# Kernel optimization log

Hardware: AMD Instinct MI355X
Metric: run time of the kernel (lower is better)

## Reference

```python
import jax, jax.numpy as jnp
import numpy as np

B, S, D = 256, 512, 128
NQ, NC, NQD, NCD = 20000, 2000, 101, 101


def setup_inputs() -> dict:
    key = jax.random.key(0)
    ks = jax.random.split(key, 32)
    s = 0.05
    inp = {
        "question_seq": jax.random.randint(ks[0], (B, S), 0, NQ),
        "concept_seq": jax.random.randint(ks[1], (B, S), 0, NC),
        "question_diff_seq": jax.random.randint(ks[2], (B, S), 0, NQD),
        "concept_diff_seq": jax.random.randint(ks[3], (B, S), 0, NCD),
        "correct_seq": jax.random.randint(ks[4], (B, S), 0, 2),
        "E_q": jax.random.normal(ks[5], (NQ, D)) * s,
        "E_c": jax.random.normal(ks[6], (NC, D)) * s,
        "E_qd": jax.random.normal(ks[7], (NQD, D)) * s,
        "E_cd": jax.random.normal(ks[8], (NCD, D)) * s,
        "E_corr": jax.random.normal(ks[9], (2, D)) * s,
        "Wx": jax.random.normal(ks[10], (4 * D, D)) * s,
        "bx": jnp.zeros((D,)),
        "W_s1": jax.random.normal(ks[11], (D, D)) * s,
        "b_s1": jnp.zeros((D,)),
        "W_s2": jax.random.normal(ks[12], (D, D)) * s,
        "b_s2": jnp.zeros((D,)),
        "W_p1": jax.random.normal(ks[13], (2 * D, D)) * s,
        "b_p1": jnp.zeros((D,)),
        "W_p2": jax.random.normal(ks[14], (2 * D, D)) * s,
        "b_p2": jnp.zeros((D,)),
        "W_ki": jax.random.normal(ks[15], (4 * D, D)) * s,
        "b_ki": jnp.zeros((D,)),
        # xavier_uniform init of h_pre: bound = sqrt(6/(fan_in+fan_out))
        "h0": jax.random.uniform(ks[16], (B, D), minval=-1.0, maxval=1.0) * np.sqrt(6.0 / (B + D)),
    }
    return inp


def reference(question_seq, concept_seq, question_diff_seq, concept_diff_seq,
              correct_seq, E_q, E_c, E_qd, E_cd, E_corr,
              Wx, bx, W_s1, b_s1, W_s2, b_s2,
              W_p1, b_p1, W_p2, b_p2, W_ki, b_ki, h0):
    # embedding lookups: [B,S,D] each
    q = E_q[question_seq]
    c = E_c[concept_seq]
    qd = E_qd[question_diff_seq]
    cd = E_cd[concept_diff_seq]
    corr = E_corr[correct_seq]
    # generate_x_MLP applied to full sequence at once (loop-invariant)
    x = jnp.concatenate([q, c, qd, cd], axis=-1) @ Wx + bx  # [B,S,D]
    # time-major inputs for the recurrence over t = 0..S-2
    xs = jnp.swapaxes(x, 0, 1)          # [S,B,D]
    corr_t = jnp.swapaxes(corr, 0, 1)   # [S,B,D]
    qd_t = jnp.swapaxes(qd, 0, 1)
    cd_t = jnp.swapaxes(cd, 0, 1)

    def step(h, inp):
        x_t, x_next, co, qdt, cdt = inp
        d = x_t - h
        sdf = jax.nn.sigmoid(d @ W_s1 + b_s1) * jnp.tanh(d @ W_s2 + b_s2)  # dropout=eval
        pk_in = jnp.concatenate([sdf, co], axis=-1)
        pka = jax.nn.sigmoid(pk_in @ W_p1 + b_p1) * jnp.tanh(pk_in @ W_p2 + b_p2)
        ki_in = jnp.concatenate([h, co, qdt, cdt], axis=-1)
        g = jax.nn.sigmoid(ki_in @ W_ki + b_ki)
        h_new = g * h + (1.0 - g) * pka
        y_t = jax.nn.sigmoid(jnp.sum(x_next * h_new, axis=-1))  # [B]
        return h_new, y_t

    scan_in = (xs[:-1], xs[1:], corr_t[:-1], qd_t[:-1], cd_t[:-1])
    _, y_body = jax.lax.scan(step, h0, scan_in)  # y_body: [S-1,B]
    y = jnp.concatenate([y_body.T, jnp.zeros((question_seq.shape[0], 1), y_body.dtype)], axis=1)
    return y  # [B,S], last column zero as in original
```

## Files before the change

### kernel.cpp

```cpp
#include <hip/hip_runtime.h>

#define BB 256
#define SS 512
#define DD 128

__device__ __forceinline__ float sigf(float v) {
    return __builtin_amdgcn_rcpf(1.0f + __expf(-v));
}
__device__ __forceinline__ float tanhf_(float v) {
    return 1.0f - 2.0f * __builtin_amdgcn_rcpf(__expf(2.0f * v) + 1.0f);
}

__device__ __forceinline__ void lds_barrier() {
    asm volatile("s_waitcnt lgkmcnt(0)" ::: "memory");
    __builtin_amdgcn_s_barrier();
    __builtin_amdgcn_sched_barrier(0);
}

typedef _Float16 f16x2 __attribute__((ext_vector_type(2)));
typedef _Float16 f16x8 __attribute__((ext_vector_type(8)));
typedef float    f32x4 __attribute__((ext_vector_type(4)));

#define MFMA16(A, B, C) __builtin_amdgcn_mfma_f32_16x16x32_f16((A), (B), (C), 0, 0, 0)

#define N_EQ  (20000 * 128)
#define N_EC  (2000 * 128)
#define N_EQD (101 * 128)
#define N_ECD (101 * 128)
#define N_WXT (512 * 128)
#define N_WS  (128 * 128)
#define N_CVT (N_EQ + N_EC + N_EQD + N_ECD + N_WXT + 2 * N_WS)

__global__ __launch_bounds__(256) void dimkt_cvt(
    const float* __restrict__ E_q, const float* __restrict__ E_c,
    const float* __restrict__ E_qd, const float* __restrict__ E_cd,
    const float* __restrict__ Wx,
    const float* __restrict__ W_s1, const float* __restrict__ W_s2,
    _Float16* __restrict__ E_qh, _Float16* __restrict__ E_ch,
    _Float16* __restrict__ E_qdh, _Float16* __restrict__ E_cdh,
    _Float16* __restrict__ WxTh,
    _Float16* __restrict__ Ws1T, _Float16* __restrict__ Ws2T)
{
    int o = blockIdx.x * 256 + threadIdx.x;
    if (o >= N_CVT) return;
    if (o < N_EQ) { E_qh[o] = (_Float16)E_q[o]; return; }
    o -= N_EQ;
    if (o < N_EC) { E_ch[o] = (_Float16)E_c[o]; return; }
    o -= N_EC;
    if (o < N_EQD) { E_qdh[o] = (_Float16)E_qd[o]; return; }
    o -= N_EQD;
    if (o < N_ECD) { E_cdh[o] = (_Float16)E_cd[o]; return; }
    o -= N_ECD;
    if (o < N_WXT) {
        int n = o >> 9, k = o & 511;
        WxTh[o] = (_Float16)Wx[k * 128 + n];
        return;
    }
    o -= N_WXT;
    if (o < N_WS) {
        int n = o >> 7, k = o & 127;
        Ws1T[o] = (_Float16)W_s1[k * 128 + n];
        return;
    }
    o -= N_WS;
    {
        int n = o >> 7, k = o & 127;
        Ws2T[o] = (_Float16)W_s2[k * 128 + n];
    }
}

__global__ void dimkt_tables(const float* __restrict__ E_corr,
                             const float* __restrict__ E_qd,
                             const float* __restrict__ E_cd,
                             const float* __restrict__ W_ki,
                             const float* __restrict__ W_p1,
                             const float* __restrict__ W_p2,
                             const float* __restrict__ b_ki,
                             const float* __restrict__ b_p1,
                             const float* __restrict__ b_p2,
                             float* __restrict__ Ck, float* __restrict__ Cp1,
                             float* __restrict__ Cp2, float* __restrict__ Qk,
                             float* __restrict__ Cdk)
{
    __shared__ float e[128];
    const int r = blockIdx.x;
    const int j = threadIdx.x;
    const float *emb, *W, *bias;
    float* op;
    if (r < 2)        { emb = E_corr + r * 128;        W = W_ki + 128 * 128; bias = b_ki;    op = Ck  + r * 128; }
    else if (r < 4)   { emb = E_corr + (r - 2) * 128;  W = W_p1 + 128 * 128; bias = b_p1;    op = Cp1 + (r - 2) * 128; }
    else if (r < 6)   { emb = E_corr + (r - 4) * 128;  W = W_p2 + 128 * 128; bias = b_p2;    op = Cp2 + (r - 4) * 128; }
    else if (r < 107) { emb = E_qd   + (r - 6) * 128;  W = W_ki + 256 * 128; bias = nullptr; op = Qk  + (r - 6) * 128; }
    else              { emb = E_cd   + (r - 107) * 128; W = W_ki + 384 * 128; bias = nullptr; op = Cdk + (r - 107) * 128; }
    e[j] = emb[j];
    __syncthreads();
    float acc = bias ? bias[j] : 0.0f;
#pragma unroll 8
    for (int i = 0; i < 128; ++i) acc = fmaf(e[i], W[i * 128 + j], acc);
    op[j] = acc;
}

__global__ __launch_bounds__(256, 2) void dimkt_xgemm(
    const int* __restrict__ q_seq, const int* __restrict__ c_seq,
    const int* __restrict__ qd_seq, const int* __restrict__ cd_seq,
    const _Float16* __restrict__ E_qh, const _Float16* __restrict__ E_ch,
    const _Float16* __restrict__ E_qdh, const _Float16* __restrict__ E_cdh,
    const _Float16* __restrict__ WxTh,
    const float* __restrict__ bx, _Float16* __restrict__ xh)
{
    const int tid = threadIdx.x;
    const int wv  = tid >> 6;
    const int l   = tid & 63;
    const int lm  = l & 15;
    const int kg8 = (l >> 4) * 8;
    const int m0  = blockIdx.x * 128;
    const int rbase = m0 + wv * 32;

    f32x4 acc0[8], acc1[8];
#pragma unroll
    for (int c = 0; c < 8; ++c) {
        acc0[c] = (f32x4){0.f, 0.f, 0.f, 0.f};
        acc1[c] = (f32x4){0.f, 0.f, 0.f, 0.f};
    }

#pragma unroll
    for (int s = 0; s < 4; ++s) {
        const _Float16* T  = (s == 0) ? E_qh : (s == 1) ? E_ch : (s == 2) ? E_qdh : E_cdh;
        const int*      sq = (s == 0) ? q_seq : (s == 1) ? c_seq : (s == 2) ? qd_seq : cd_seq;
        const int i0 = sq[rbase + lm];
        const int i1 = sq[rbase + 16 + lm];
        const _Float16* a0p = T + (size_t)i0 * 128 + kg8;
        const _Float16* a1p = T + (size_t)i1 * 128 + kg8;
#pragma unroll
        for (int kk = 0; kk < 4; ++kk) {
            const f16x8 a0 = *(const f16x8*)(a0p + kk * 32);
            const f16x8 a1 = *(const f16x8*)(a1p + kk * 32);
#pragma unroll
            for (int c = 0; c < 8; ++c) {
                const f16x8 bf = *(const f16x8*)&WxTh[(size_t)(c * 16 + lm) * 512
                                                      + s * 128 + kk * 32 + kg8];
                acc0[c] = MFMA16(a0, bf, acc0[c]);
                acc1[c] = MFMA16(a1, bf, acc1[c]);
            }
        }
    }

#pragma unroll
    for (int c = 0; c < 8; ++c) {
        const int col = c * 16 + lm;
        const float bxv = bx[col];
#pragma unroll
        for (int r = 0; r < 4; ++r) {
            const int row0 = rbase + (l >> 4) * 4 + r;
            xh[(size_t)row0 * 128 + col]        = (_Float16)(acc0[c][r] + bxv);
            xh[(size_t)(row0 + 16) * 128 + col] = (_Float16)(acc1[c][r] + bxv);
        }
    }
}

__global__ __launch_bounds__(256, 2) void dimkt_x12(
    const _Float16* __restrict__ xh,
    const _Float16* __restrict__ Ws1T, const _Float16* __restrict__ Ws2T,
    const float* __restrict__ b_s1, const float* __restrict__ b_s2,
    _Float16* __restrict__ X1h, _Float16* __restrict__ X2h)
{
    const int tid = threadIdx.x;
    const int wv  = tid >> 6;
    const int l   = tid & 63;
    const int lm  = l & 15;
    const int kg8 = (l >> 4) * 8;
    const int rbase = blockIdx.x * 128 + wv * 32;

    f32x4 acc0[16], acc1[16];
#pragma unroll
    for (int c = 0; c < 16; ++c) {
        acc0[c] = (f32x4){0.f, 0.f, 0.f, 0.f};
        acc1[c] = (f32x4){0.f, 0.f, 0.f, 0.f};
    }

    const _Float16* a0p = xh + (size_t)(rbase + lm) * 128 + kg8;
    const _Float16* a1p = xh + (size_t)(rbase + 16 + lm) * 128 + kg8;
#pragma unroll
    for (int kk = 0; kk < 4; ++kk) {
        const f16x8 a0 = *(const f16x8*)(a0p + kk * 32);
        const f16x8 a1 = *(const f16x8*)(a1p + kk * 32);
#pragma unroll
        for (int c = 0; c < 16; ++c) {
            const _Float16* BT = (c < 8) ? Ws1T : Ws2T;
            const f16x8 bf = *(const f16x8*)&BT[(size_t)((c & 7) * 16 + lm) * 128
                                                + kk * 32 + kg8];
            acc0[c] = MFMA16(a0, bf, acc0[c]);
            acc1[c] = MFMA16(a1, bf, acc1[c]);
        }
    }

#pragma unroll
    for (int c = 0; c < 16; ++c) {
        const int col = (c & 7) * 16 + lm;
        const float bv = (c < 8) ? b_s1[col] : b_s2[col];
        _Float16* ob = (c < 8) ? X1h : X2h;
#pragma unroll
        for (int r = 0; r < 4; ++r) {
            const int row0 = rbase + (l >> 4) * 4 + r;
            ob[(size_t)row0 * 128 + col]        = (_Float16)(acc0[c][r] + bv);
            ob[(size_t)(row0 + 16) * 128 + col] = (_Float16)(acc1[c][r] + bv);
        }
    }
}

__device__ __forceinline__ f16x8 load_wfrag(const float* __restrict__ W,
                                            int kbase, int j) {
    f16x8 r;
#pragma unroll
    for (int e = 0; e < 8; ++e) r[e] = (_Float16)W[(kbase + e) * DD + j];
    return r;
}

__global__ __launch_bounds__(512, 2) void dimkt_scan(
    const _Float16* __restrict__ X1h, const _Float16* __restrict__ X2h,
    const int* __restrict__ corr_seq, const int* __restrict__ qd_seq,
    const int* __restrict__ cd_seq,
    const float* __restrict__ W_s1, const float* __restrict__ W_s2,
    const float* __restrict__ W_p1, const float* __restrict__ W_p2,
    const float* __restrict__ W_ki,
    const float* __restrict__ Ck, const float* __restrict__ Cp1,
    const float* __restrict__ Cp2, const float* __restrict__ Qk,
    const float* __restrict__ Cdk,
    const float* __restrict__ h0, _Float16* __restrict__ hb,
    float* __restrict__ out)
{
    __shared__ __align__(16) _Float16 h_h[128];
    __shared__ __align__(16) _Float16 s_h[128];

    const int tid  = threadIdx.x;
    const int b    = blockIdx.x;
    const int wv   = tid >> 6;
    const int l    = tid & 63;
    const int kgrp = l >> 4;
    const int j    = wv * 16 + (l & 15);
    const int base = b * SS;

    const int kb = kgrp * 8;
    const f16x8 w1f0 = load_wfrag(W_s1,  0 + kb, j);
    const f16x8 w1f1 = load_wfrag(W_s1, 32 + kb, j);
    const f16x8 w1f2 = load_wfrag(W_s1, 64 + kb, j);
    const f16x8 w1f3 = load_wfrag(W_s1, 96 + kb, j);
    const f16x8 w2f0 = load_wfrag(W_s2,  0 + kb, j);
    const f16x8 w2f1 = load_wfrag(W_s2, 32 + kb, j);
    const f16x8 w2f2 = load_wfrag(W_s2, 64 + kb, j);
    const f16x8 w2f3 = load_wfrag(W_s2, 96 + kb, j);
    const f16x8 wkf0 = load_wfrag(W_ki,  0 + kb, j);
    const f16x8 wkf1 = load_wfrag(W_ki, 32 + kb, j);
    const f16x8 wkf2 = load_wfrag(W_ki, 64 + kb, j);
    const f16x8 wkf3 = load_wfrag(W_ki, 96 + kb, j);
    const f16x8 p1f0 = load_wfrag(W_p1,  0 + kb, j);
    const f16x8 p1f1 = load_wfrag(W_p1, 32 + kb, j);
    const f16x8 p1f2 = load_wfrag(W_p1, 64 + kb, j);
    const f16x8 p1f3 = load_wfrag(W_p1, 96 + kb, j);
    const f16x8 p2f0 = load_wfrag(W_p2,  0 + kb, j);
    const f16x8 p2f1 = load_wfrag(W_p2, 32 + kb, j);
    const f16x8 p2f2 = load_wfrag(W_p2, 64 + kb, j);
    const f16x8 p2f3 = load_wfrag(W_p2, 96 + kb, j);

    float h = h0[b * DD + j];
    if (kgrp == 0) h_h[j] = (_Float16)h;

    int ic = __builtin_amdgcn_readfirstlane(corr_seq[base]);
    int iq = __builtin_amdgcn_readfirstlane(qd_seq[base]);
    int ie = __builtin_amdgcn_readfirstlane(cd_seq[base]);
    float tck = Ck [ic * DD + j];
    float tqk = Qk [iq * DD + j];
    float tcd = Cdk[ie * DD + j];
    float tp1 = Cp1[ic * DD + j];
    float tp2 = Cp2[ic * DD + j];
    int icN = __builtin_amdgcn_readfirstlane(corr_seq[base + 1]);
    int iqN = __builtin_amdgcn_readfirstlane(qd_seq[base + 1]);
    int ieN = __builtin_amdgcn_readfirstlane(cd_seq[base + 1]);
    float X1v = (float)X1h[(size_t)base * DD + j];
    float X2v = (float)X2h[(size_t)base * DD + j];
    lds_barrier();

    for (int t = 0; t < 511; ++t) {
        float nck = Ck [icN * DD + j];
        float nqk = Qk [iqN * DD + j];
        float ncd = Cdk[ieN * DD + j];
        float np1 = Cp1[icN * DD + j];
        float np2 = Cp2[icN * DD + j];
        const int n2 = base + ((t + 2 > 511) ? 511 : (t + 2));
        int icN2 = __builtin_amdgcn_readfirstlane(corr_seq[n2]);
        int iqN2 = __builtin_amdgcn_readfirstlane(qd_seq[n2]);
        int ieN2 = __builtin_amdgcn_readfirstlane(cd_seq[n2]);
        float nX1 = (float)X1h[(size_t)(base + t + 1) * DD + j];
        float nX2 = (float)X2h[(size_t)(base + t + 1) * DD + j];

        const f16x8 hA0 = *(const f16x8*)&h_h[ 0 + kb];
        const f16x8 hA1 = *(const f16x8*)&h_h[32 + kb];
        const f16x8 hA2 = *(const f16x8*)&h_h[64 + kb];
        const f16x8 hA3 = *(const f16x8*)&h_h[96 + kb];

        const f32x4 z = {0.f, 0.f, 0.f, 0.f};
        f32x4 c1a = MFMA16(hA0, w1f0, z);
        f32x4 c2a = MFMA16(hA0, w2f0, z);
        f32x4 cka = MFMA16(hA0, wkf0, z);
        f32x4 c1b = MFMA16(hA2, w1f2, z);
        f32x4 c2b = MFMA16(hA2, w2f2, z);
        f32x4 ckb = MFMA16(hA2, wkf2, z);
        c1a = MFMA16(hA1, w1f1, c1a);
        c2a = MFMA16(hA1, w2f1, c2a);
        cka = MFMA16(hA1, wkf1, cka);
        c1b = MFMA16(hA3, w1f3, c1b);
        c2b = MFMA16(hA3, w2f3, c2b);
        ckb = MFMA16(hA3, wkf3, ckb);

        float a1 = X1v - (c1a[0] + c1b[0]);
        float a2 = X2v - (c2a[0] + c2b[0]);
        float kg = cka[0] + ckb[0] + tck + tqk + tcd;
        float sdf = sigf(a1) * tanhf_(a2);
        float g   = sigf(kg);
        if (kgrp == 0) s_h[j] = (_Float16)sdf;
        lds_barrier();

        const f16x8 sA0 = *(const f16x8*)&s_h[ 0 + kb];
        const f16x8 sA1 = *(const f16x8*)&s_h[32 + kb];
        const f16x8 sA2 = *(const f16x8*)&s_h[64 + kb];
        const f16x8 sA3 = *(const f16x8*)&s_h[96 + kb];

        f32x4 q1a = MFMA16(sA0, p1f0, z);
        f32x4 q2a = MFMA16(sA0, p2f0, z);
        f32x4 q1b = MFMA16(sA2, p1f2, z);
        f32x4 q2b = MFMA16(sA2, p2f2, z);
        q1a = MFMA16(sA1, p1f1, q1a);
        q2a = MFMA16(sA1, p2f1, q2a);
        q1b = MFMA16(sA3, p1f3, q1b);
        q2b = MFMA16(sA3, p2f3, q2b);

        float pka = sigf(q1a[0] + q1b[0] + tp1) * tanhf_(q2a[0] + q2b[0] + tp2);
        float hn  = fmaf(g, h - pka, pka);
        _Float16 hn16 = (_Float16)hn;
        if (kgrp == 0) {
            h_h[j] = hn16;
            hb[(size_t)(base + t) * DD + j] = hn16;
        }

        h = hn;
        X1v = nX1; X2v = nX2;
        tck = nck; tqk = nqk; tcd = ncd; tp1 = np1; tp2 = np2;
        icN = icN2; iqN = iqN2; ieN = ieN2;
        lds_barrier();
    }

    if (tid == 0) out[base + 511] = 0.0f;
}

__global__ __launch_bounds__(256) void dimkt_y(
    const _Float16* __restrict__ xh, const _Float16* __restrict__ hb,
    float* __restrict__ out)
{
    const int o = blockIdx.x * 4 + (threadIdx.x >> 6);
    const int l = threadIdx.x & 63;
    const int b = o >> 9;
    const int t = o & 511;
    if (t == 511) return;
    f16x2 xv = *(const f16x2*)&xh[((size_t)(b * SS + t + 1)) * DD + 2 * l];
    f16x2 hv = *(const f16x2*)&hb[((size_t)(b * SS + t)) * DD + 2 * l];
    float s = (float)xv.x * (float)hv.x + (float)xv.y * (float)hv.y;
    s += __shfl_xor(s, 1);  s += __shfl_xor(s, 2);  s += __shfl_xor(s, 4);
    s += __shfl_xor(s, 8);  s += __shfl_xor(s, 16); s += __shfl_xor(s, 32);
    if (l == 0) out[b * SS + t] = sigf(s);
}

extern "C" void kernel_launch(void* const* d_in, const int* in_sizes, int n_in,
                              void* d_out, int out_size, void* d_ws, size_t ws_size,
                              hipStream_t stream) {
    const int*   q_seq    = (const int*)d_in[0];
    const int*   c_seq    = (const int*)d_in[1];
    const int*   qd_seq   = (const int*)d_in[2];
    const int*   cd_seq   = (const int*)d_in[3];
    const int*   corr_seq = (const int*)d_in[4];
    const float* E_q    = (const float*)d_in[5];
    const float* E_c    = (const float*)d_in[6];
    const float* E_qd   = (const float*)d_in[7];
    const float* E_cd   = (const float*)d_in[8];
    const float* E_corr = (const float*)d_in[9];
    const float* Wx     = (const float*)d_in[10];
    const float* bx     = (const float*)d_in[11];
    const float* W_s1   = (const float*)d_in[12];
    const float* b_s1   = (const float*)d_in[13];
    const float* W_s2   = (const float*)d_in[14];
    const float* b_s2   = (const float*)d_in[15];
    const float* W_p1   = (const float*)d_in[16];
    const float* b_p1   = (const float*)d_in[17];
    const float* W_p2   = (const float*)d_in[18];
    const float* b_p2   = (const float*)d_in[19];
    const float* W_ki   = (const float*)d_in[20];
    const float* b_ki   = (const float*)d_in[21];
    const float* h0     = (const float*)d_in[22];
    float* out = (float*)d_out;

    float* Ck   = (float*)d_ws;
    float* Cp1  = Ck  + 256;
    float* Cp2  = Cp1 + 256;
    float* Qk   = Cp2 + 256;
    float* Cdk  = Qk  + 101 * 128;
    _Float16* pool  = (_Float16*)((char*)d_ws + (size_t)131072);
    const size_t NBT = (size_t)BB * SS * DD;
    _Float16* xh    = pool;
    _Float16* X1h   = xh  + NBT;
    _Float16* X2h   = X1h + NBT;
    _Float16* hbuf  = X2h + NBT;
    _Float16* E_qh  = hbuf + NBT;
    _Float16* E_ch  = E_qh + N_EQ;
    _Float16* E_qdh = E_ch + N_EC;
    _Float16* E_cdh = E_qdh + N_EQD;
    _Float16* WxTh  = E_cdh + N_ECD;
    _Float16* Ws1T  = WxTh + N_WXT;
    _Float16* Ws2T  = Ws1T + N_WS;

    dimkt_cvt<<<(N_CVT + 255) / 256, 256, 0, stream>>>(
        E_q, E_c, E_qd, E_cd, Wx, W_s1, W_s2,
        E_qh, E_ch, E_qdh, E_cdh, WxTh, Ws1T, Ws2T);

    dimkt_tables<<<208, 128, 0, stream>>>(E_corr, E_qd, E_cd, W_ki, W_p1, W_p2,
                                          b_ki, b_p1, b_p2, Ck, Cp1, Cp2, Qk, Cdk);

    dimkt_xgemm<<<(BB * SS) / 128, 256, 0, stream>>>(q_seq, c_seq, qd_seq, cd_seq,
                                                     E_qh, E_ch, E_qdh, E_cdh,
                                                     WxTh, bx, xh);

    dimkt_x12<<<(BB * SS) / 128, 256, 0, stream>>>(xh, Ws1T, Ws2T, b_s1, b_s2,
                                                   X1h, X2h);

    dimkt_scan<<<BB, 512, 0, stream>>>(X1h, X2h, corr_seq, qd_seq, cd_seq,
                                       W_s1, W_s2, W_p1, W_p2, W_ki,
                                       Ck, Cp1, Cp2, Qk, Cdk, h0, hbuf, out);

    dimkt_y<<<(BB * SS) / 4, 256, 0, stream>>>(xh, hbuf, out);
}
```

Baseline: 541.2 us.

## Halve scan block to 4 waves, each computing two 16-column tiles

The recurrent scan kernel now runs with 256 threads (4 waves) per batch row instead of 512, and each wave handles two 16-column output tiles, holding twice as many weight fragments in registers. Fewer waves means cheaper block-wide barriers on the two LDS syncs per timestep and more independent MFMAs per wave to hide latency. The cost is higher register pressure (40 f16x8 weight fragments per lane) and less parallelism per block, which the 256 blocks on a large GPU may not offset.

```diff
diff --git a/kernel.cpp b/kernel.cpp
--- a/kernel.cpp
+++ b/kernel.cpp
@@ -216,7 +216,7 @@
     return r;
 }
 
-__global__ __launch_bounds__(512, 2) void dimkt_scan(
+__global__ __launch_bounds__(256, 1) void dimkt_scan(
     const _Float16* __restrict__ X1h, const _Float16* __restrict__ X2h,
     const int* __restrict__ corr_seq, const int* __restrict__ qd_seq,
     const int* __restrict__ cd_seq,
@@ -237,87 +237,110 @@
     const int wv   = tid >> 6;
     const int l    = tid & 63;
     const int kgrp = l >> 4;
-    const int j    = wv * 16 + (l & 15);
+    const int kb   = kgrp * 8;
+    const int j0   = wv * 32 + (l & 15);
+    const int j1   = j0 + 16;
     const int base = b * SS;
 
-    const int kb = kgrp * 8;
-    const f16x8 w1f0 = load_wfrag(W_s1,  0 + kb, j);
-    const f16x8 w1f1 = load_wfrag(W_s1, 32 + kb, j);
-    const f16x8 w1f2 = load_wfrag(W_s1, 64 + kb, j);
-    const f16x8 w1f3 = load_wfrag(W_s1, 96 + kb, j);
-    const f16x8 w2f0 = load_wfrag(W_s2,  0 + kb, j);
-    const f16x8 w2f1 = load_wfrag(W_s2, 32 + kb, j);
-    const f16x8 w2f2 = load_wfrag(W_s2, 64 + kb, j);
-    const f16x8 w2f3 = load_wfrag(W_s2, 96 + kb, j);
-    const f16x8 wkf0 = load_wfrag(W_ki,  0 + kb, j);
-    const f16x8 wkf1 = load_wfrag(W_ki, 32 + kb, j);
-    const f16x8 wkf2 = load_wfrag(W_ki, 64 + kb, j);
-    const f16x8 wkf3 = load_wfrag(W_ki, 96 + kb, j);
-    const f16x8 p1f0 = load_wfrag(W_p1,  0 + kb, j);
-    const f16x8 p1f1 = load_wfrag(W_p1, 32 + kb, j);
-    const f16x8 p1f2 = load_wfrag(W_p1, 64 + kb, j);
-    const f16x8 p1f3 = load_wfrag(W_p1, 96 + kb, j);
-    const f16x8 p2f0 = load_wfrag(W_p2,  0 + kb, j);
-    const f16x8 p2f1 = load_wfrag(W_p2, 32 + kb, j);
-    const f16x8 p2f2 = load_wfrag(W_p2, 64 + kb, j);
-    const f16x8 p2f3 = load_wfrag(W_p2, 96 + kb, j);
-
-    float h = h0[b * DD + j];
-    if (kgrp == 0) h_h[j] = (_Float16)h;
+    f16x8 w1[2][4], w2[2][4], wk[2][4], p1[2][4], p2[2][4];
+#pragma unroll
+    for (int ct = 0; ct < 2; ++ct) {
+        const int col = ct ? j1 : j0;
+#pragma unroll
+        for (int kf = 0; kf < 4; ++kf) {
+            const int kbase = kf * 32 + kb;
+            w1[ct][kf] = load_wfrag(W_s1, kbase, col);
+            w2[ct][kf] = load_wfrag(W_s2, kbase, col);
+            wk[ct][kf] = load_wfrag(W_ki, kbase, col);
+            p1[ct][kf] = load_wfrag(W_p1, kbase, col);
+            p2[ct][kf] = load_wfrag(W_p2, kbase, col);
+        }
+    }
+
+    float h0v = h0[b * DD + j0];
+    float h1v = h0[b * DD + j1];
+    if (kgrp == 0) {
+        h_h[j0] = (_Float16)h0v;
+        h_h[j1] = (_Float16)h1v;
+    }
 
     int ic = __builtin_amdgcn_readfirstlane(corr_seq[base]);
     int iq = __builtin_amdgcn_readfirstlane(qd_seq[base]);
     int ie = __builtin_amdgcn_readfirstlane(cd_seq[base]);
-    float tck = Ck [ic * DD + j];
-    float tqk = Qk [iq * DD + j];
-    float tcd = Cdk[ie * DD + j];
-    float tp1 = Cp1[ic * DD + j];
-    float tp2 = Cp2[ic * DD + j];
+    float tck0 = Ck [ic * DD + j0], tck1 = Ck [ic * DD + j1];
+    float tqk0 = Qk [iq * DD + j0], tqk1 = Qk [iq * DD + j1];
+    float tcd0 = Cdk[ie * DD + j0], tcd1 = Cdk[ie * DD + j1];
+    float tp10 = Cp1[ic * DD + j0], tp11 = Cp1[ic * DD + j1];
+    float tp20 = Cp2[ic * DD + j0], tp21 = Cp2[ic * DD + j1];
     int icN = __builtin_amdgcn_readfirstlane(corr_seq[base + 1]);
     int iqN = __builtin_amdgcn_readfirstlane(qd_seq[base + 1]);
     int ieN = __builtin_amdgcn_readfirstlane(cd_seq[base + 1]);
-    float X1v = (float)X1h[(size_t)base * DD + j];
-    float X2v = (float)X2h[(size_t)base * DD + j];
+    float X1v0 = (float)X1h[(size_t)base * DD + j0];
+    float X1v1 = (float)X1h[(size_t)base * DD + j1];
+    float X2v0 = (float)X2h[(size_t)base * DD + j0];
+    float X2v1 = (float)X2h[(size_t)base * DD + j1];
     lds_barrier();
 
+    const f32x4 z = {0.f, 0.f, 0.f, 0.f};
+
     for (int t = 0; t < 511; ++t) {
-        float nck = Ck [icN * DD + j];
-        float nqk = Qk [iqN * DD + j];
-        float ncd = Cdk[ieN * DD + j];
-        float np1 = Cp1[icN * DD + j];
-        float np2 = Cp2[icN * DD + j];
+        float nck0 = Ck [icN * DD + j0], nck1 = Ck [icN * DD + j1];
+        float nqk0 = Qk [iqN * DD + j0], nqk1 = Qk [iqN * DD + j1];
+        float ncd0 = Cdk[ieN * DD + j0], ncd1 = Cdk[ieN * DD + j1];
+        float np10 = Cp1[icN * DD + j0], np11 = Cp1[icN * DD + j1];
+        float np20 = Cp2[icN * DD + j0], np21 = Cp2[icN * DD + j1];
         const int n2 = base + ((t + 2 > 511) ? 511 : (t + 2));
         int icN2 = __builtin_amdgcn_readfirstlane(corr_seq[n2]);
         int iqN2 = __builtin_amdgcn_readfirstlane(qd_seq[n2]);
         int ieN2 = __builtin_amdgcn_readfirstlane(cd_seq[n2]);
-        float nX1 = (float)X1h[(size_t)(base + t + 1) * DD + j];
-        float nX2 = (float)X2h[(size_t)(base + t + 1) * DD + j];
+        const size_t xoff = (size_t)(base + t + 1) * DD;
+        float nX10 = (float)X1h[xoff + j0];
+        float nX11 = (float)X1h[xoff + j1];
+        float nX20 = (float)X2h[xoff + j0];
+        float nX21 = (float)X2h[xoff + j1];
 
         const f16x8 hA0 = *(const f16x8*)&h_h[ 0 + kb];
         const f16x8 hA1 = *(const f16x8*)&h_h[32 + kb];
         const f16x8 hA2 = *(const f16x8*)&h_h[64 + kb];
         const f16x8 hA3 = *(const f16x8*)&h_h[96 + kb];
 
-        const f32x4 z = {0.f, 0.f, 0.f, 0.f};
-        f32x4 c1a = MFMA16(hA0, w1f0, z);
-        f32x4 c2a = MFMA16(hA0, w2f0, z);
-        f32x4 cka = MFMA16(hA0, wkf0, z);
-        f32x4 c1b = MFMA16(hA2, w1f2, z);
-        f32x4 c2b = MFMA16(hA2, w2f2, z);
-        f32x4 ckb = MFMA16(hA2, wkf2, z);
-        c1a = MFMA16(hA1, w1f1, c1a);
-        c2a = MFMA16(hA1, w2f1, c2a);
-        cka = MFMA16(hA1, wkf1, cka);
-        c1b = MFMA16(hA3, w1f3, c1b);
-        c2b = MFMA16(hA3, w2f3, c2b);
-        ckb = MFMA16(hA3, wkf3, ckb);
-
-        float a1 = X1v - (c1a[0] + c1b[0]);
-        float a2 = X2v - (c2a[0] + c2b[0]);
-        float kg = cka[0] + ckb[0] + tck + tqk + tcd;
-        float sdf = sigf(a1) * tanhf_(a2);
-        float g   = sigf(kg);
-        if (kgrp == 0) s_h[j] = (_Float16)sdf;
+        f32x4 c1a0 = MFMA16(hA0, w1[0][0], z);
+        f32x4 c1b0 = MFMA16(hA2, w1[0][2], z);
+        f32x4 c2a0 = MFMA16(hA0, w2[0][0], z);
+        f32x4 c2b0 = MFMA16(hA2, w2[0][2], z);
+        f32x4 cka0 = MFMA16(hA0, wk[0][0], z);
+        f32x4 ckb0 = MFMA16(hA2, wk[0][2], z);
+        f32x4 c1a1 = MFMA16(hA0, w1[1][0], z);
+        f32x4 c1b1 = MFMA16(hA2, w1[1][2], z);
+        f32x4 c2a1 = MFMA16(hA0, w2[1][0], z);
+        f32x4 c2b1 = MFMA16(hA2, w2[1][2], z);
+        f32x4 cka1 = MFMA16(hA0, wk[1][0], z);
+        f32x4 ckb1 = MFMA16(hA2, wk[1][2], z);
+        c1a0 = MFMA16(hA1, w1[0][1], c1a0);
+        c1b0 = MFMA16(hA3, w1[0][3], c1b0);
+        c2a0 = MFMA16(hA1, w2[0][1], c2a0);
+        c2b0 = MFMA16(hA3, w2[0][3], c2b0);
+        cka0 = MFMA16(hA1, wk[0][1], cka0);
+        ckb0 = MFMA16(hA3, wk[0][3], ckb0);
+        c1a1 = MFMA16(hA1, w1[1][1], c1a1);
+        c1b1 = MFMA16(hA3, w1[1][3], c1b1);
+        c2a1 = MFMA16(hA1, w2[1][1], c2a1);
+        c2b1 = MFMA16(hA3, w2[1][3], c2b1);
+        cka1 = MFMA16(hA1, wk[1][1], cka1);
+        ckb1 = MFMA16(hA3, wk[1][3], ckb1);
+
+        float a10 = X1v0 - (c1a0[0] + c1b0[0]);
+        float a20 = X2v0 - (c2a0[0] + c2b0[0]);
+        float a11 = X1v1 - (c1a1[0] + c1b1[0]);
+        float a21 = X2v1 - (c2a1[0] + c2b1[0]);
+        float sdf0 = sigf(a10) * tanhf_(a20);
+        float sdf1 = sigf(a11) * tanhf_(a21);
+        if (kgrp == 0) {
+            s_h[j0] = (_Float16)sdf0;
+            s_h[j1] = (_Float16)sdf1;
+        }
+        float g0 = sigf(cka0[0] + ckb0[0] + tck0 + tqk0 + tcd0);
+        float g1 = sigf(cka1[0] + ckb1[0] + tck1 + tqk1 + tcd1);
         lds_barrier();
 
         const f16x8 sA0 = *(const f16x8*)&s_h[ 0 + kb];
@@ -325,26 +348,43 @@
         const f16x8 sA2 = *(const f16x8*)&s_h[64 + kb];
         const f16x8 sA3 = *(const f16x8*)&s_h[96 + kb];
 
-        f32x4 q1a = MFMA16(sA0, p1f0, z);
-        f32x4 q2a = MFMA16(sA0, p2f0, z);
-        f32x4 q1b = MFMA16(sA2, p1f2, z);
-        f32x4 q2b = MFMA16(sA2, p2f2, z);
-        q1a = MFMA16(sA1, p1f1, q1a);
-        q2a = MFMA16(sA1, p2f1, q2a);
-        q1b = MFMA16(sA3, p1f3, q1b);
-        q2b = MFMA16(sA3, p2f3, q2b);
-
-        float pka = sigf(q1a[0] + q1b[0] + tp1) * tanhf_(q2a[0] + q2b[0] + tp2);
-        float hn  = fmaf(g, h - pka, pka);
-        _Float16 hn16 = (_Float16)hn;
+        f32x4 q1a0 = MFMA16(sA0, p1[0][0], z);
+        f32x4 q1b0 = MFMA16(sA2, p1[0][2], z);
+        f32x4 q2a0 = MFMA16(sA0, p2[0][0], z);
+        f32x4 q2b0 = MFMA16(sA2, p2[0][2], z);
+        f32x4 q1a1 = MFMA16(sA0, p1[1][0], z);
+        f32x4 q1b1 = MFMA16(sA2, p1[1][2], z);
+        f32x4 q2a1 = MFMA16(sA0, p2[1][0], z);
+        f32x4 q2b1 = MFMA16(sA2, p2[1][2], z);
+        q1a0 = MFMA16(sA1, p1[0][1], q1a0);
+        q1b0 = MFMA16(sA3, p1[0][3], q1b0);
+        q2a0 = MFMA16(sA1, p2[0][1], q2a0);
+        q2b0 = MFMA16(sA3, p2[0][3], q2b0);
+        q1a1 = MFMA16(sA1, p1[1][1], q1a1);
+        q1b1 = MFMA16(sA3, p1[1][3], q1b1);
+        q2a1 = MFMA16(sA1, p2[1][1], q2a1);
+        q2b1 = MFMA16(sA3, p2[1][3], q2b1);
+
+        float pka0 = sigf(q1a0[0] + q1b0[0] + tp10) * tanhf_(q2a0[0] + q2b0[0] + tp20);
+        float pka1 = sigf(q1a1[0] + q1b1[0] + tp11) * tanhf_(q2a1[0] + q2b1[0] + tp21);
+        float hn0 = fmaf(g0, h0v - pka0, pka0);
+        float hn1 = fmaf(g1, h1v - pka1, pka1);
+        _Float16 hn016 = (_Float16)hn0;
+        _Float16 hn116 = (_Float16)hn1;
         if (kgrp == 0) {
-            h_h[j] = hn16;
-            hb[(size_t)(base + t) * DD + j] = hn16;
-        }
-
-        h = hn;
-        X1v = nX1; X2v = nX2;
-        tck = nck; tqk = nqk; tcd = ncd; tp1 = np1; tp2 = np2;
+            h_h[j0] = hn016;
+            h_h[j1] = hn116;
+        }
+        if (kgrp == 0) {
+            hb[(size_t)(base + t) * DD + j0] = hn016;
+            hb[(size_t)(base + t) * DD + j1] = hn116;
+        }
+
+        h0v = hn0; h1v = hn1;
+        X1v0 = nX10; X1v1 = nX11; X2v0 = nX20; X2v1 = nX21;
+        tck0 = nck0; tck1 = nck1; tqk0 = nqk0; tqk1 = nqk1;
+        tcd0 = ncd0; tcd1 = ncd1; tp10 = np10; tp11 = np11;
+        tp20 = np20; tp21 = np21;
         icN = icN2; iqN = iqN2; ieN = ieN2;
         lds_barrier();
     }
@@ -430,7 +470,7 @@
     dimkt_x12<<<(BB * SS) / 128, 256, 0, stream>>>(xh, Ws1T, Ws2T, b_s1, b_s2,
                                                    X1h, X2h);
 
-    dimkt_scan<<<BB, 512, 0, stream>>>(X1h, X2h, corr_seq, qd_seq, cd_seq,
+    dimkt_scan<<<BB, 256, 0, stream>>>(X1h, X2h, corr_seq, qd_seq, cd_seq,
                                        W_s1, W_s2, W_p1, W_p2, W_ki,
                                        Ck, Cp1, Cp2, Qk, Cdk, h0, hbuf, out);
 
```

New measurement: 640.9 us. 1.18x slower.
